# Kernel tuning notes

Hardware: AMD Instinct MI355X
Metric: run time of the kernel (lower is better)

Reference implementation:

```python
import jax
import jax.numpy as jnp
from jax import lax
import numpy as np

B, ND, H, W = 8, 8, 512, 512
CONF = 0.9
MARGIN = 3.0
MIN_CLUSTER = 50
MAX_X = 102.4
MPP0, MPP1 = 0.2, 0.2
K = 32  # max clusters (torch version grows an unbounded python list)


def setup_inputs() -> dict:
    key = jax.random.key(0)
    k1, k2, k3, k4, k5, k6 = jax.random.split(key, 6)
    return {
        "seg": jax.random.uniform(k1, (B, 1, H, W), dtype=jnp.float32),
        "embedding": jax.random.normal(k2, (B, ND, H, W), dtype=jnp.float32),
        "offset_pred": jax.random.normal(k3, (B, 1, H, W), dtype=jnp.float32),
        "z_pred": jax.random.normal(k4, (B, 1, H, W), dtype=jnp.float32),
        "intrinsic": jax.random.normal(k5, (B, 3, 3), dtype=jnp.float32),
        "extrinsic": jax.random.normal(k6, (B, 4, 4), dtype=jnp.float32),
    }


def _cluster_one(seg_flat, emb_flat):
    # seg_flat: [N], emb_flat: [N, ND]. Greedy sequential embedding clustering
    # (naive_cluster_nd): running-mean centers, assign to nearest center if
    # within MARGIN else open a new one. Fixed K slots; counts>0 marks active.
    nd = emb_flat.shape[1]

    def step(carry, xs):
        centers, counts = carry  # [K, nd], [K]
        s, e = xs
        valid = s >= CONF
        d = jnp.sqrt(jnp.sum((centers - e) ** 2, axis=1))
        d = jnp.where(counts > 0, d, jnp.inf)
        cid_min = jnp.argmin(d).astype(jnp.int32)
        join = d[cid_min] < MARGIN
        n_active = jnp.sum(counts > 0).astype(jnp.int32)
        cid = jnp.where(join, cid_min, jnp.minimum(n_active, K - 1))
        cnt = counts[cid]
        new_c = jnp.where(join, (centers[cid] * cnt + e) / (cnt + 1.0), e)
        centers = jnp.where(valid, centers.at[cid].set(new_c), centers)
        counts = jnp.where(valid, counts.at[cid].add(1.0), counts)
        return (centers, counts), jnp.where(valid, cid, -1)

    init = (jnp.zeros((K, nd), emb_flat.dtype), jnp.zeros((K,), emb_flat.dtype))
    (_, _), cids = lax.scan(step, init, (seg_flat, emb_flat))
    return cids  # [N] int32, -1 = background


def reference(seg, embedding, offset_pred, z_pred, intrinsic, extrinsic):
    b, nd, h, w = embedding.shape
    seg_flat = seg[:, 0].reshape(b, h * w)
    emb_flat = embedding.reshape(b, nd, h * w).transpose(0, 2, 1)  # [B, N, nd]
    cids = jax.vmap(_cluster_one)(seg_flat, emb_flat).reshape(b, h, w)
    lanes = jnp.where(cids >= 0, cids + 1, 0)  # [B, H, W], 0 = background

    # mean_col_by_row_with_offset_z: per (batch, lane, row) mean of col+offset and z
    offset_y = jax.nn.sigmoid(offset_pred[:, 0])          # [B, H, W]
    x_adj = jnp.arange(w, dtype=seg.dtype)[None, None, :] + offset_y
    zc = z_pred[:, 0]
    b_idx = jnp.arange(b)[:, None, None]
    h_idx = jnp.arange(h)[None, :, None]
    seg_ids = ((b_idx * (K + 1) + lanes) * h + h_idx).reshape(-1)
    num = b * (K + 1) * h

    def ssum(v):
        return jax.ops.segment_sum(v.reshape(-1), seg_ids, num_segments=num).reshape(b, K + 1, h)[:, 1:]

    cnt = ssum(jnp.ones((b, h, w), seg.dtype))            # [B, K, H]
    mean_x = ssum(x_adj) / jnp.maximum(cnt, 1.0)
    mean_z = ssum(zc) / jnp.maximum(cnt, 1.0)

    size = cnt.sum(-1)                                    # cluster pixel count
    n_rows = (cnt > 0).sum(-1)                            # rows per lane
    valid = (cnt > 0) & (size[:, :, None] >= MIN_CLUSTER) & (n_rows[:, :, None] >= 2)

    # ego-coordinate transform from forward()
    x_world = (MAX_X / MPP0 - (jnp.arange(h, dtype=seg.dtype) + 0.5)) * MPP0  # [H]
    x_world = jnp.broadcast_to(x_world, (b, K, h))
    y_world = -(mean_x - (w // 2)) * MPP1
    points = jnp.stack([x_world, y_world, mean_z], axis=1)  # [B, 3, K, H]
    points = jnp.where(valid[:, None], points, 0.0)
    return points, valid
```

## Files before the change

kernel.cpp:

```cpp
#include <hip/hip_runtime.h>

#define HW_ (512 * 512)
#define B_ 8
#define H_ 512
#define W_ 512
#define K_ 32
#define CH_ 16
#define CHPIX_ (HW_ / CH_)

__global__ void k_count(const float* __restrict__ seg, int* __restrict__ chunkCnt) {
  const int blk = blockIdx.x;
  const int t = threadIdx.x;
  const float4* __restrict__ s4 = (const float4*)(seg + (size_t)blk * CHPIX_) + (size_t)t * 16;
  int cnt = 0;
#pragma unroll
  for (int j = 0; j < 16; ++j) {
    float4 v = s4[j];
    cnt += (v.x >= 0.9f) + (v.y >= 0.9f) + (v.z >= 0.9f) + (v.w >= 0.9f);
  }
  __shared__ int red[256];
  red[t] = cnt;
  __syncthreads();
  for (int off = 128; off > 0; off >>= 1) {
    if (t < off) red[t] += red[t + off];
    __syncthreads();
  }
  if (t == 0) chunkCnt[blk] = red[0];
}

__global__ void k_scan(const int* __restrict__ chunkCnt, int* __restrict__ chunkBase,
                       int* __restrict__ nvalid, int cap) {
  const int t = threadIdx.x;
  if (t < B_ * CH_) {
    const int b = t / CH_, c = t % CH_;
    int base = 0;
    for (int q = 0; q < c; ++q) base += chunkCnt[b * CH_ + q];
    chunkBase[t] = base;
    if (c == CH_ - 1) nvalid[b] = min(base + chunkCnt[t], cap);
  }
}

__global__ void k_fill(const float* __restrict__ seg, const float* __restrict__ emb,
                       const int* __restrict__ chunkBase, unsigned char* __restrict__ lanes,
                       int* __restrict__ idxC, float* __restrict__ embC, int cap) {
  const int blk = blockIdx.x;
  const int b = blk / CH_;
  const int t = threadIdx.x;
  const size_t pixbase = (size_t)blk * CHPIX_ + (size_t)t * 64;
  const float4* __restrict__ s4 = (const float4*)(seg + pixbase);

  int cnt = 0;
#pragma unroll
  for (int j = 0; j < 16; ++j) {
    float4 v = s4[j];
    cnt += (v.x >= 0.9f) + (v.y >= 0.9f) + (v.z >= 0.9f) + (v.w >= 0.9f);
  }
  __shared__ int pre[256];
  pre[t] = cnt;
  __syncthreads();
  for (int off = 1; off < 256; off <<= 1) {
    int mine = pre[t];
    int add = (t >= off) ? pre[t - off] : 0;
    __syncthreads();
    pre[t] = mine + add;
    __syncthreads();
  }
  int w = chunkBase[blk] + pre[t] - cnt;

  uint4 z = {0u, 0u, 0u, 0u};
  uint4* lz = (uint4*)(lanes + pixbase);
  lz[0] = z; lz[1] = z; lz[2] = z; lz[3] = z;

  const float* __restrict__ eb = emb + (size_t)b * 8 * HW_;
  const int pixInB = (int)(pixbase - (size_t)b * HW_);
  for (int j = 0; j < 16; ++j) {
    float4 v = s4[j];
    float sv[4] = {v.x, v.y, v.z, v.w};
#pragma unroll
    for (int q = 0; q < 4; ++q) {
      if (sv[q] >= 0.9f && w < cap) {
        const int p = pixInB + j * 4 + q;
        idxC[(size_t)b * cap + w] = p;
        float* dst = embC + ((size_t)b * cap + w) * 8;
#pragma unroll
        for (int dd = 0; dd < 8; ++dd) dst[dd] = eb[(size_t)dd * HW_ + p];
        ++w;
      }
    }
  }
}


#define TILE_ 32

__device__ __forceinline__ void stage16(const float* g, float* l) {
  __builtin_amdgcn_global_load_lds(
      (const __attribute__((address_space(1))) void*)g,
      (__attribute__((address_space(3))) void*)l, 16, 0, 0);
}

#define RLF(V, L) __uint_as_float((unsigned)__builtin_amdgcn_readlane(__float_as_int(V), (L)))

#define STEPP(J)                                                                     \
  do {                                                                               \
    const float e0 = RLF(td.x, 2 * (J)), e1 = RLF(td.y, 2 * (J));                    \
    const float e2 = RLF(td.z, 2 * (J)), e3 = RLF(td.w, 2 * (J));                    \
    const float e4 = RLF(td.x, 2 * (J) + 1), e5 = RLF(td.y, 2 * (J) + 1);            \
    const float e6 = RLF(td.z, 2 * (J) + 1), e7 = RLF(td.w, 2 * (J) + 1);            \
    float t0 = C0 - e0, t1 = C1 - e1, t2 = C2 - e2, t3 = C3 - e3;                    \
    float t4 = C4 - e4, t5 = C5 - e5, t6 = C6 - e6, t7 = C7 - e7;                    \
    float a0 = t0 * t0 + t1 * t1;                                                    \
    float a1 = t2 * t2 + t3 * t3;                                                    \
    float a2 = t4 * t4 + t5 * t5;                                                    \
    float a3 = t6 * t6 + t7 * t7;                                                    \
    float dsq = (a0 + a1) + (a2 + a3);                                               \
    unsigned db = __float_as_uint(dsq);                                              \
    unsigned dbm = db > emptyBits ? db : emptyBits;         \
    unsigned key = (dbm & 0xFFFFFFE0u) | (unsigned)cl;             \
    unsigned mn = key, mr;                                                           \
    mr = (unsigned)__builtin_amdgcn_update_dpp(0, (int)mn, 0xB1, 0xF, 0xF, true);    \
    mn = mn < mr ? mn : mr;                                                          \
    mr = (unsigned)__builtin_amdgcn_update_dpp(0, (int)mn, 0x4E, 0xF, 0xF, true);    \
    mn = mn < mr ? mn : mr;                                                          \
    mr = (unsigned)__builtin_amdgcn_update_dpp(0, (int)mn, 0x141, 0xF, 0xF, true);   \
    mn = mn < mr ? mn : mr;                                                          \
    mr = (unsigned)__builtin_amdgcn_update_dpp(0, (int)mn, 0x140, 0xF, 0xF, true);   \
    mn = mn < mr ? mn : mr;                                                          \
    unsigned q0 = (unsigned)__builtin_amdgcn_readlane((int)mn, 0);                   \
    unsigned q1 = (unsigned)__builtin_amdgcn_readlane((int)mn, 16);                  \
    unsigned mv = q0 < q1 ? q0 : q1;                            \
    bool join = mv < 0x41100000u;            \
    int cid = join ? (int)(mv & 31u) : (nact < 31 ? nact : 31);                      \
    nact += join ? 0 : 1;                                                            \
    bool own = (cl == cid);                                                          \
    float wj = join ? inv : 1.0f;                                                    \
    float w = own ? wj : 0.0f;                                                       \
    C0 = __builtin_fmaf(t0, -w, C0);                                                 \
    C1 = __builtin_fmaf(t1, -w, C1);                                                 \
    C2 = __builtin_fmaf(t2, -w, C2);                                                 \
    C3 = __builtin_fmaf(t3, -w, C3);                                                 \
    C4 = __builtin_fmaf(t4, -w, C4);                                                 \
    C5 = __builtin_fmaf(t5, -w, C5);                                                 \
    C6 = __builtin_fmaf(t6, -w, C6);                                                 \
    C7 = __builtin_fmaf(t7, -w, C7);                                                 \
    cnt += own ? 1.0f : 0.0f;                                                        \
    inv = __builtin_amdgcn_rcpf(cnt + 1.0f);          \
    emptyBits = own ? 0u : emptyBits;                                                \
    pk |= (unsigned long long)(unsigned)(cid + 1) << (((J) & 7) * 8);                \
    if (((J) & 7) == 7) {                                                            \
      if (lane == 0) *(unsigned long long*)(cptr + ((J) & ~7)) = pk;                 \
      pk = 0ULL;                                                                     \
    }                                                                                \
  } while (0)

__global__ __launch_bounds__(64, 1) void k_cluster(const float* __restrict__ embC,
                                                   const int* __restrict__ nvalid,
                                                   unsigned char* __restrict__ cidArr,
                                                   int cap) {
  __shared__ float lds[512];
  const int b = blockIdx.x;
  const int lane = threadIdx.x;
  const int cl = lane & 31;
  const int n = nvalid[b];
  if (n <= 0) return;
  const int nTiles = (n + TILE_ - 1) / TILE_;

  const float* src = embC + (size_t)b * cap * 8 + lane * 4;
  unsigned char* cidB = cidArr + (size_t)b * HW_;

  float C0 = 0.f, C1 = 0.f, C2 = 0.f, C3 = 0.f, C4 = 0.f, C5 = 0.f, C6 = 0.f, C7 = 0.f;
  float cnt = 0.f, inv = 1.0f;
  unsigned emptyBits = 0x7F800000u;
  int nact = 0;
  unsigned long long pk = 0ULL;

  stage16(src, lds);
  asm volatile("s_waitcnt vmcnt(0)" ::: "memory");
  __builtin_amdgcn_sched_barrier(0);
  float4 td = ((const float4*)lds)[lane];

  for (int ti = 0; ti < nTiles; ++ti) {
    unsigned char* cptr = cidB + ti * TILE_;
    if (ti + 1 < nTiles)
      stage16(src + (size_t)(ti + 1) * 256, lds + ((ti + 1) & 1) * 128);

    STEPP(0);  STEPP(1);  STEPP(2);  STEPP(3);
    STEPP(4);  STEPP(5);  STEPP(6);  STEPP(7);
    STEPP(8);  STEPP(9);  STEPP(10); STEPP(11);
    STEPP(12); STEPP(13); STEPP(14); STEPP(15);
    STEPP(16); STEPP(17); STEPP(18); STEPP(19);
    STEPP(20); STEPP(21); STEPP(22); STEPP(23);
    STEPP(24); STEPP(25); STEPP(26); STEPP(27);
    STEPP(28); STEPP(29); STEPP(30); STEPP(31);

    if (ti + 1 < nTiles) {
      asm volatile("s_waitcnt vmcnt(4)" ::: "memory");
      __builtin_amdgcn_sched_barrier(0);
      td = ((const float4*)(lds + ((ti + 1) & 1) * 128))[lane];
    }
  }
}

__global__ void k_scatter(const unsigned char* __restrict__ cidArr,
                          const int* __restrict__ idxC, const int* __restrict__ nvalid,
                          unsigned char* __restrict__ lanes, int cap) {
  const int b = blockIdx.y;
  const int n = nvalid[b];
  for (int j = blockIdx.x * blockDim.x + threadIdx.x; j < n; j += gridDim.x * blockDim.x) {
    lanes[(size_t)b * HW_ + idxC[(size_t)b * cap + j]] = cidArr[(size_t)b * HW_ + j];
  }
}

__global__ void k_rowsum(const unsigned char* __restrict__ lanes,
                         const float* __restrict__ offp, const float* __restrict__ zp,
                         float* __restrict__ cnt, float* __restrict__ sx,
                         float* __restrict__ sz) {
  const int bh = blockIdx.x;
  const int b = bh >> 9, h = bh & 511;
  __shared__ float sc[33], sxx[33], szz[33];
  const int t = threadIdx.x;
  if (t < 33) { sc[t] = 0.f; sxx[t] = 0.f; szz[t] = 0.f; }
  __syncthreads();
  const size_t base = (size_t)bh * W_;
  for (int x = t; x < W_; x += 256) {
    int ln = lanes[base + x];
    float o = offp[base + x];
    float sig = 1.0f / (1.0f + expf(-o));
    float xa = (float)x + sig;
    float zv = zp[base + x];
    atomicAdd(&sc[ln], 1.0f);
    atomicAdd(&sxx[ln], xa);
    atomicAdd(&szz[ln], zv);
  }
  __syncthreads();
  if (t >= 1 && t < 33) {
    size_t o = ((size_t)b * K_ + (t - 1)) * H_ + h;
    cnt[o] = sc[t]; sx[o] = sxx[t]; sz[o] = szz[t];
  }
}

__global__ void k_final(const float* __restrict__ cnt, const float* __restrict__ sx,
                        const float* __restrict__ sz, float* __restrict__ out) {
  const int bk = blockIdx.x;
  const int b = bk >> 5, k = bk & 31;
  const int h = threadIdx.x;
  const size_t o = (size_t)bk * H_ + h;
  float c = cnt[o];
  float sc_ = c, sn = (c > 0.f) ? 1.f : 0.f;
#pragma unroll
  for (int off = 32; off >= 1; off >>= 1) {
    sc_ += __shfl_down(sc_, off);
    sn += __shfl_down(sn, off);
  }
  __shared__ float rs[8], rn[8], tot[2];
  const int wid = h >> 6, lid = h & 63;
  if (lid == 0) { rs[wid] = sc_; rn[wid] = sn; }
  __syncthreads();
  if (h == 0) {
    float a = 0, bb = 0;
#pragma unroll
    for (int q = 0; q < 8; ++q) { a += rs[q]; bb += rn[q]; }
    tot[0] = a; tot[1] = bb;
  }
  __syncthreads();
  float size = tot[0], nrows = tot[1];
  bool valid = (c > 0.f) && (size >= 50.f) && (nrows >= 2.f);
  float mx = sx[o] / fmaxf(c, 1.f);
  float mz = sz[o] / fmaxf(c, 1.f);
  float xw = (512.0f - ((float)h + 0.5f)) * 0.2f;
  float yw = -(mx - 256.0f) * 0.2f;
  out[((size_t)(b * 3 + 0) * K_ + k) * H_ + h] = valid ? xw : 0.f;
  out[((size_t)(b * 3 + 1) * K_ + k) * H_ + h] = valid ? yw : 0.f;
  out[((size_t)(b * 3 + 2) * K_ + k) * H_ + h] = valid ? mz : 0.f;
  out[(size_t)B_ * 3 * K_ * H_ + (size_t)bk * H_ + h] = valid ? 1.f : 0.f;
}

extern "C" void kernel_launch(void* const* d_in, const int* in_sizes, int n_in,
                              void* d_out, int out_size, void* d_ws, size_t ws_size,
                              hipStream_t stream) {
  const float* seg  = (const float*)d_in[0];
  const float* emb  = (const float*)d_in[1];
  const float* offp = (const float*)d_in[2];
  const float* zp   = (const float*)d_in[3];
  float* out = (float*)d_out;
  char* ws = (char*)d_ws;

  const size_t lanesOff = 0;
  const size_t cntOff   = (size_t)B_ * HW_;
  const size_t sxOff    = cntOff + (size_t)B_ * K_ * H_ * 4;
  const size_t szOff    = sxOff  + (size_t)B_ * K_ * H_ * 4;
  const size_t nvOff    = szOff  + (size_t)B_ * K_ * H_ * 4;
  const size_t ccOff    = nvOff + 256;
  const size_t cbOff    = ccOff + 1024;
  const size_t cidOff   = cbOff + 1024;
  const size_t idxOff   = cidOff + (size_t)B_ * HW_;
  size_t avail = (ws_size > idxOff + 4096) ? (ws_size - idxOff - 4096) : 0;
  long long capLL = (long long)(avail / ((size_t)B_ * 36));
  if (capLL > (long long)HW_) capLL = HW_;
  if (capLL < 1) capLL = 1;
  const int cap = (int)capLL;
  const size_t embOff = idxOff + (size_t)B_ * cap * 4;

  unsigned char* lanes = (unsigned char*)(ws + lanesOff);
  float* cnt = (float*)(ws + cntOff);
  float* sx  = (float*)(ws + sxOff);
  float* sz  = (float*)(ws + szOff);
  int* nvalid = (int*)(ws + nvOff);
  int* chunkCnt  = (int*)(ws + ccOff);
  int* chunkBase = (int*)(ws + cbOff);
  unsigned char* cidArr = (unsigned char*)(ws + cidOff);
  int* idxC   = (int*)(ws + idxOff);
  float* embC = (float*)(ws + embOff);

  k_count<<<B_ * CH_, 256, 0, stream>>>(seg, chunkCnt);
  k_scan<<<1, 128, 0, stream>>>(chunkCnt, chunkBase, nvalid, cap);
  k_fill<<<B_ * CH_, 256, 0, stream>>>(seg, emb, chunkBase, lanes, idxC, embC, cap);
  k_cluster<<<B_, 64, 0, stream>>>(embC, nvalid, cidArr, cap);
  k_scatter<<<dim3(64, B_), 256, 0, stream>>>(cidArr, idxC, nvalid, lanes, cap);
  k_rowsum<<<B_ * H_, 256, 0, stream>>>(lanes, offp, zp, cnt, sx, sz);
  k_final<<<B_ * K_, H_, 0, stream>>>(cnt, sx, sz, out);
}
```

Measured before the change: 3.119 ms.

## Pack two batches per wave in clustering kernel with fused DPP min reduction

The greedy clustering kernel now processes two batch images in one 64-lane wave: each 32-lane half holds the cluster centers for one image, and the grid shrinks from eight blocks to four. The cross-lane min reduction is rewritten in inline assembly as fused v_min_u32_dpp instructions, aiming to shorten the serial per-pixel dependency chain. Tiles shrink to 16 pixels per phase, and each step does twice as many readlanes plus per-half selects. Each wave now runs for the longer of its two images, and the shorter image computes on padding data past its end.

```diff
diff --git a/kernel.cpp b/kernel.cpp
--- a/kernel.cpp
+++ b/kernel.cpp
@@ -91,7 +91,7 @@
 }
 
 
-#define TILE_ 32
+#define PHPX_ 16
 
 __device__ __forceinline__ void stage16(const float* g, float* l) {
   __builtin_amdgcn_global_load_lds(
@@ -100,57 +100,78 @@
 }
 
 #define RLF(V, L) __uint_as_float((unsigned)__builtin_amdgcn_readlane(__float_as_int(V), (L)))
-
-#define STEPP(J)                                                                     \
-  do {                                                                               \
-    const float e0 = RLF(td.x, 2 * (J)), e1 = RLF(td.y, 2 * (J));                    \
-    const float e2 = RLF(td.z, 2 * (J)), e3 = RLF(td.w, 2 * (J));                    \
-    const float e4 = RLF(td.x, 2 * (J) + 1), e5 = RLF(td.y, 2 * (J) + 1);            \
-    const float e6 = RLF(td.z, 2 * (J) + 1), e7 = RLF(td.w, 2 * (J) + 1);            \
-    float t0 = C0 - e0, t1 = C1 - e1, t2 = C2 - e2, t3 = C3 - e3;                    \
-    float t4 = C4 - e4, t5 = C5 - e5, t6 = C6 - e6, t7 = C7 - e7;                    \
-    float a0 = t0 * t0 + t1 * t1;                                                    \
-    float a1 = t2 * t2 + t3 * t3;                                                    \
-    float a2 = t4 * t4 + t5 * t5;                                                    \
-    float a3 = t6 * t6 + t7 * t7;                                                    \
-    float dsq = (a0 + a1) + (a2 + a3);                                               \
-    unsigned db = __float_as_uint(dsq);                                              \
-    unsigned dbm = db > emptyBits ? db : emptyBits;         \
-    unsigned key = (dbm & 0xFFFFFFE0u) | (unsigned)cl;             \
-    unsigned mn = key, mr;                                                           \
-    mr = (unsigned)__builtin_amdgcn_update_dpp(0, (int)mn, 0xB1, 0xF, 0xF, true);    \
-    mn = mn < mr ? mn : mr;                                                          \
-    mr = (unsigned)__builtin_amdgcn_update_dpp(0, (int)mn, 0x4E, 0xF, 0xF, true);    \
-    mn = mn < mr ? mn : mr;                                                          \
-    mr = (unsigned)__builtin_amdgcn_update_dpp(0, (int)mn, 0x141, 0xF, 0xF, true);   \
-    mn = mn < mr ? mn : mr;                                                          \
-    mr = (unsigned)__builtin_amdgcn_update_dpp(0, (int)mn, 0x140, 0xF, 0xF, true);   \
-    mn = mn < mr ? mn : mr;                                                          \
-    unsigned q0 = (unsigned)__builtin_amdgcn_readlane((int)mn, 0);                   \
-    unsigned q1 = (unsigned)__builtin_amdgcn_readlane((int)mn, 16);                  \
-    unsigned mv = q0 < q1 ? q0 : q1;                            \
-    bool join = mv < 0x41100000u;            \
-    int cid = join ? (int)(mv & 31u) : (nact < 31 ? nact : 31);                      \
-    nact += join ? 0 : 1;                                                            \
-    bool own = (cl == cid);                                                          \
-    float wj = join ? inv : 1.0f;                                                    \
-    float w = own ? wj : 0.0f;                                                       \
-    C0 = __builtin_fmaf(t0, -w, C0);                                                 \
-    C1 = __builtin_fmaf(t1, -w, C1);                                                 \
-    C2 = __builtin_fmaf(t2, -w, C2);                                                 \
-    C3 = __builtin_fmaf(t3, -w, C3);                                                 \
-    C4 = __builtin_fmaf(t4, -w, C4);                                                 \
-    C5 = __builtin_fmaf(t5, -w, C5);                                                 \
-    C6 = __builtin_fmaf(t6, -w, C6);                                                 \
-    C7 = __builtin_fmaf(t7, -w, C7);                                                 \
-    cnt += own ? 1.0f : 0.0f;                                                        \
-    inv = __builtin_amdgcn_rcpf(cnt + 1.0f);          \
-    emptyBits = own ? 0u : emptyBits;                                                \
-    pk |= (unsigned long long)(unsigned)(cid + 1) << (((J) & 7) * 8);                \
-    if (((J) & 7) == 7) {                                                            \
-      if (lane == 0) *(unsigned long long*)(cptr + ((J) & ~7)) = pk;                 \
-      pk = 0ULL;                                                                     \
-    }                                                                                \
+#define RLU(V, L) ((unsigned)__builtin_amdgcn_readlane((int)(V), (L)))
+
+#define PSTEP(J)                                                                   \
+  do {                                                                             \
+    const float eA0 = RLF(td.x, 2 * (J)), eA1 = RLF(td.y, 2 * (J));                \
+    const float eA2 = RLF(td.z, 2 * (J)), eA3 = RLF(td.w, 2 * (J));                \
+    const float eA4 = RLF(td.x, 2 * (J) + 1), eA5 = RLF(td.y, 2 * (J) + 1);        \
+    const float eA6 = RLF(td.z, 2 * (J) + 1), eA7 = RLF(td.w, 2 * (J) + 1);        \
+    const float eB0 = RLF(td.x, 32 + 2 * (J)), eB1 = RLF(td.y, 32 + 2 * (J));      \
+    const float eB2 = RLF(td.z, 32 + 2 * (J)), eB3 = RLF(td.w, 32 + 2 * (J));      \
+    const float eB4 = RLF(td.x, 33 + 2 * (J)), eB5 = RLF(td.y, 33 + 2 * (J));      \
+    const float eB6 = RLF(td.z, 33 + 2 * (J)), eB7 = RLF(td.w, 33 + 2 * (J));      \
+    float t0 = hi ? (C0 - eB0) : (C0 - eA0);                                       \
+    float t1 = hi ? (C1 - eB1) : (C1 - eA1);                                       \
+    float t2 = hi ? (C2 - eB2) : (C2 - eA2);                                       \
+    float t3 = hi ? (C3 - eB3) : (C3 - eA3);                                       \
+    float t4 = hi ? (C4 - eB4) : (C4 - eA4);                                       \
+    float t5 = hi ? (C5 - eB5) : (C5 - eA5);                                       \
+    float t6 = hi ? (C6 - eB6) : (C6 - eA6);                                       \
+    float t7 = hi ? (C7 - eB7) : (C7 - eA7);                                       \
+    float a0 = t0 * t0 + t1 * t1;                                                  \
+    float a1 = t2 * t2 + t3 * t3;                                                  \
+    float a2 = t4 * t4 + t5 * t5;                                                  \
+    float a3 = t6 * t6 + t7 * t7;                                                  \
+    float dsq = (a0 + a1) + (a2 + a3);                                             \
+    unsigned db = __float_as_uint(dsq);                                            \
+    unsigned dbm = db > emptyBits ? db : emptyBits;       \
+    unsigned mn = (dbm & 0xFFFFFFE0u) | (unsigned)cl;                              \
+    asm volatile(                                                                  \
+        "s_nop 1\n\t"                                                              \
+        "v_min_u32_dpp %0, %0, %0 quad_perm:[1,0,3,2] row_mask:0xf bank_mask:0xf\n\t" \
+        "s_nop 1\n\t"                                                              \
+        "v_min_u32_dpp %0, %0, %0 quad_perm:[2,3,0,1] row_mask:0xf bank_mask:0xf\n\t" \
+        "s_nop 1\n\t"                                                              \
+        "v_min_u32_dpp %0, %0, %0 row_half_mirror row_mask:0xf bank_mask:0xf\n\t"  \
+        "s_nop 1\n\t"                                                              \
+        "v_min_u32_dpp %0, %0, %0 row_mirror row_mask:0xf bank_mask:0xf\n\t"       \
+        "s_nop 1"                                                                  \
+        : "+v"(mn));                                                               \
+    unsigned q0 = RLU(mn, 0), q1 = RLU(mn, 16);                                    \
+    unsigned q2 = RLU(mn, 32), q3 = RLU(mn, 48);                                   \
+    unsigned mvA = q0 < q1 ? q0 : q1;                         \
+    unsigned mvB = q2 < q3 ? q2 : q3;                                              \
+    bool joinA = mvA < 0x41100000u;               \
+    bool joinB = mvB < 0x41100000u;                                                \
+    int cidA = joinA ? (int)(mvA & 31u) : (nactA < 31 ? nactA : 31);               \
+    int cidB = joinB ? (int)(mvB & 31u) : (nactB < 31 ? nactB : 31);               \
+    nactA += joinA ? 0 : 1;                                                        \
+    nactB += joinB ? 0 : 1;                                                        \
+    bool own = (cl == (hi ? cidB : cidA));                                         \
+    bool join_my = hi ? joinB : joinA;                                             \
+    float wj = join_my ? inv : 1.0f;                                               \
+    float w = own ? wj : 0.0f;                                                     \
+    C0 = __builtin_fmaf(t0, -w, C0);                                               \
+    C1 = __builtin_fmaf(t1, -w, C1);                                               \
+    C2 = __builtin_fmaf(t2, -w, C2);                                               \
+    C3 = __builtin_fmaf(t3, -w, C3);                                               \
+    C4 = __builtin_fmaf(t4, -w, C4);                                               \
+    C5 = __builtin_fmaf(t5, -w, C5);                                               \
+    C6 = __builtin_fmaf(t6, -w, C6);                                               \
+    C7 = __builtin_fmaf(t7, -w, C7);                                               \
+    cnt += own ? 1.0f : 0.0f;                                                      \
+    inv = __builtin_amdgcn_rcpf(cnt + 1.0f);        \
+    emptyBits = own ? 0u : emptyBits;                                              \
+    pkA |= (unsigned long long)(unsigned)(cidA + 1) << (((J) & 7) * 8);            \
+    pkB |= (unsigned long long)(unsigned)(cidB + 1) << (((J) & 7) * 8);            \
+    if (((J) & 7) == 7) {                                                          \
+      if (lane == 0) *(unsigned long long*)(cpA + ((J) & ~7)) = pkA;               \
+      if (lane == 32) *(unsigned long long*)(cpB + ((J) & ~7)) = pkB;              \
+      pkA = 0ULL;                                                                  \
+      pkB = 0ULL;                                                                  \
+    }                                                                              \
   } while (0)
 
 __global__ __launch_bounds__(64, 1) void k_cluster(const float* __restrict__ embC,
@@ -158,45 +179,46 @@
                                                    unsigned char* __restrict__ cidArr,
                                                    int cap) {
   __shared__ float lds[512];
-  const int b = blockIdx.x;
+  const int blk = blockIdx.x;
   const int lane = threadIdx.x;
+  const bool hi = lane >= 32;
   const int cl = lane & 31;
-  const int n = nvalid[b];
-  if (n <= 0) return;
-  const int nTiles = (n + TILE_ - 1) / TILE_;
-
-  const float* src = embC + (size_t)b * cap * 8 + lane * 4;
-  unsigned char* cidB = cidArr + (size_t)b * HW_;
+  const int bA = 2 * blk, bB = 2 * blk + 1;
+  const int nA = nvalid[bA], nB = nvalid[bB];
+  const int nMax = nA > nB ? nA : nB;
+  if (nMax <= 0) return;
+  const int nPh = (nMax + PHPX_ - 1) / PHPX_;
+
+  const float* gsrc = embC + (size_t)(hi ? bB : bA) * cap * 8 + (size_t)cl * 4;
+  unsigned char* cA = cidArr + (size_t)bA * HW_;
+  unsigned char* cB = cidArr + (size_t)bB * HW_;
 
   float C0 = 0.f, C1 = 0.f, C2 = 0.f, C3 = 0.f, C4 = 0.f, C5 = 0.f, C6 = 0.f, C7 = 0.f;
   float cnt = 0.f, inv = 1.0f;
   unsigned emptyBits = 0x7F800000u;
-  int nact = 0;
-  unsigned long long pk = 0ULL;
-
-  stage16(src, lds);
+  int nactA = 0, nactB = 0;
+  unsigned long long pkA = 0ULL, pkB = 0ULL;
+
+  stage16(gsrc, lds);
   asm volatile("s_waitcnt vmcnt(0)" ::: "memory");
   __builtin_amdgcn_sched_barrier(0);
   float4 td = ((const float4*)lds)[lane];
 
-  for (int ti = 0; ti < nTiles; ++ti) {
-    unsigned char* cptr = cidB + ti * TILE_;
-    if (ti + 1 < nTiles)
-      stage16(src + (size_t)(ti + 1) * 256, lds + ((ti + 1) & 1) * 128);
-
-    STEPP(0);  STEPP(1);  STEPP(2);  STEPP(3);
-    STEPP(4);  STEPP(5);  STEPP(6);  STEPP(7);
-    STEPP(8);  STEPP(9);  STEPP(10); STEPP(11);
-    STEPP(12); STEPP(13); STEPP(14); STEPP(15);
-    STEPP(16); STEPP(17); STEPP(18); STEPP(19);
-    STEPP(20); STEPP(21); STEPP(22); STEPP(23);
-    STEPP(24); STEPP(25); STEPP(26); STEPP(27);
-    STEPP(28); STEPP(29); STEPP(30); STEPP(31);
-
-    if (ti + 1 < nTiles) {
+  for (int ph = 0; ph < nPh; ++ph) {
+    unsigned char* cpA = cA + ph * PHPX_;
+    unsigned char* cpB = cB + ph * PHPX_;
+    if (ph + 1 < nPh)
+      stage16(gsrc + (size_t)(ph + 1) * 128, lds + ((ph + 1) & 1) * 256);
+
+    PSTEP(0);  PSTEP(1);  PSTEP(2);  PSTEP(3);
+    PSTEP(4);  PSTEP(5);  PSTEP(6);  PSTEP(7);
+    PSTEP(8);  PSTEP(9);  PSTEP(10); PSTEP(11);
+    PSTEP(12); PSTEP(13); PSTEP(14); PSTEP(15);
+
+    if (ph + 1 < nPh) {
       asm volatile("s_waitcnt vmcnt(4)" ::: "memory");
       __builtin_amdgcn_sched_barrier(0);
-      td = ((const float4*)(lds + ((ti + 1) & 1) * 128))[lane];
+      td = ((const float4*)(lds + ((ph + 1) & 1) * 256))[lane];
     }
   }
 }
@@ -294,10 +316,11 @@
   const size_t cbOff    = ccOff + 1024;
   const size_t cidOff   = cbOff + 1024;
   const size_t idxOff   = cidOff + (size_t)B_ * HW_;
-  size_t avail = (ws_size > idxOff + 4096) ? (ws_size - idxOff - 4096) : 0;
+  size_t avail = (ws_size > idxOff + 8192) ? (ws_size - idxOff - 8192) : 0;
   long long capLL = (long long)(avail / ((size_t)B_ * 36));
   if (capLL > (long long)HW_) capLL = HW_;
-  if (capLL < 1) capLL = 1;
+  if (capLL < 2) capLL = 2;
+  capLL &= ~1LL;
   const int cap = (int)capLL;
   const size_t embOff = idxOff + (size_t)B_ * cap * 4;
 
@@ -315,7 +338,7 @@
   k_count<<<B_ * CH_, 256, 0, stream>>>(seg, chunkCnt);
   k_scan<<<1, 128, 0, stream>>>(chunkCnt, chunkBase, nvalid, cap);
   k_fill<<<B_ * CH_, 256, 0, stream>>>(seg, emb, chunkBase, lanes, idxC, embC, cap);
-  k_cluster<<<B_, 64, 0, stream>>>(embC, nvalid, cidArr, cap);
+  k_cluster<<<B_ / 2, 64, 0, stream>>>(embC, nvalid, cidArr, cap);
   k_scatter<<<dim3(64, B_), 256, 0, stream>>>(cidArr, idxC, nvalid, lanes, cap);
   k_rowsum<<<B_ * H_, 256, 0, stream>>>(lanes, offp, zp, cnt, sx, sz);
   k_final<<<B_ * K_, H_, 0, stream>>>(cnt, sx, sz, out);
```

Measured after the change: 6.262 ms. 101% more time.

## Feed cluster embeddings via scalar loads instead of LDS staging and readlane

Applied to the files above, without the earlier changes.

The sequential clustering kernel now loads each point's 8-dim embedding straight into scalar registers with s_load_dwordx16, double-buffered eight points at a time. This replaces the global-to-LDS staging followed by per-element readlane broadcasts, removing eight readlanes and the LDS traffic from every serial step. It also flips the delta sign so the distance uses fma, and writes the packed cluster ids every eight points. The change adds prefetch reads past the valid range, so the workspace padding and an even cap are adjusted to keep them in bounds.

```diff
diff --git a/kernel.cpp b/kernel.cpp
--- a/kernel.cpp
+++ b/kernel.cpp
@@ -91,33 +91,40 @@
 }
 
 
-#define TILE_ 32
-
-__device__ __forceinline__ void stage16(const float* g, float* l) {
-  __builtin_amdgcn_global_load_lds(
-      (const __attribute__((address_space(1))) void*)g,
-      (__attribute__((address_space(3))) void*)l, 16, 0, 0);
-}
-
-#define RLF(V, L) __uint_as_float((unsigned)__builtin_amdgcn_readlane(__float_as_int(V), (L)))
-
-#define STEPP(J)                                                                     \
+typedef unsigned u32x16 __attribute__((ext_vector_type(16)));
+
+#define RLU(V, L) ((unsigned)__builtin_amdgcn_readlane((int)(V), (L)))
+
+#define SLOAD(SA, SB, OFF)                                            \
+  asm volatile("s_load_dwordx16 %0, %2, %3\n\t"                       \
+               "s_load_dwordx16 %1, %2, %4"                           \
+               : "=s"(SA), "=s"(SB)                                   \
+               : "s"(src), "s"((OFF)), "s"((OFF) + 64u));
+
+#define SWAIT(SA, SB) \
+  asm volatile("s_waitcnt lgkmcnt(0)" : "+s"(SA), "+s"(SB));
+
+#define STEPS(J, SV, BI)                                                              \
   do {                                                                               \
-    const float e0 = RLF(td.x, 2 * (J)), e1 = RLF(td.y, 2 * (J));                    \
-    const float e2 = RLF(td.z, 2 * (J)), e3 = RLF(td.w, 2 * (J));                    \
-    const float e4 = RLF(td.x, 2 * (J) + 1), e5 = RLF(td.y, 2 * (J) + 1);            \
-    const float e6 = RLF(td.z, 2 * (J) + 1), e7 = RLF(td.w, 2 * (J) + 1);            \
-    float t0 = C0 - e0, t1 = C1 - e1, t2 = C2 - e2, t3 = C3 - e3;                    \
-    float t4 = C4 - e4, t5 = C5 - e5, t6 = C6 - e6, t7 = C7 - e7;                    \
-    float a0 = t0 * t0 + t1 * t1;                                                    \
-    float a1 = t2 * t2 + t3 * t3;                                                    \
-    float a2 = t4 * t4 + t5 * t5;                                                    \
-    float a3 = t6 * t6 + t7 * t7;                                                    \
-    float dsq = (a0 + a1) + (a2 + a3);                                               \
+    const float e0 = __uint_as_float((SV)[(BI) + 0]);                                \
+    const float e1 = __uint_as_float((SV)[(BI) + 1]);                                \
+    const float e2 = __uint_as_float((SV)[(BI) + 2]);                                \
+    const float e3 = __uint_as_float((SV)[(BI) + 3]);                                \
+    const float e4 = __uint_as_float((SV)[(BI) + 4]);                                \
+    const float e5 = __uint_as_float((SV)[(BI) + 5]);                                \
+    const float e6 = __uint_as_float((SV)[(BI) + 6]);                                \
+    const float e7 = __uint_as_float((SV)[(BI) + 7]);                                \
+    float t0 = e0 - C0, t1 = e1 - C1, t2 = e2 - C2, t3 = e3 - C3;                    \
+    float t4 = e4 - C4, t5 = e5 - C5, t6 = e6 - C6, t7 = e7 - C7;                    \
+    float m0 = t0 * t0; m0 = __builtin_fmaf(t1, t1, m0);                             \
+    float m1 = t2 * t2; m1 = __builtin_fmaf(t3, t3, m1);                             \
+    float m2 = t4 * t4; m2 = __builtin_fmaf(t5, t5, m2);                             \
+    float m3 = t6 * t6; m3 = __builtin_fmaf(t7, t7, m3);                             \
+    float dsq = (m0 + m1) + (m2 + m3);                                               \
     unsigned db = __float_as_uint(dsq);                                              \
     unsigned dbm = db > emptyBits ? db : emptyBits;         \
-    unsigned key = (dbm & 0xFFFFFFE0u) | (unsigned)cl;             \
-    unsigned mn = key, mr;                                                           \
+    unsigned mn = (dbm & 0xFFFFFFE0u) | (unsigned)cl;      \
+    unsigned mr;                                                                     \
     mr = (unsigned)__builtin_amdgcn_update_dpp(0, (int)mn, 0xB1, 0xF, 0xF, true);    \
     mn = mn < mr ? mn : mr;                                                          \
     mr = (unsigned)__builtin_amdgcn_update_dpp(0, (int)mn, 0x4E, 0xF, 0xF, true);    \
@@ -126,8 +133,7 @@
     mn = mn < mr ? mn : mr;                                                          \
     mr = (unsigned)__builtin_amdgcn_update_dpp(0, (int)mn, 0x140, 0xF, 0xF, true);   \
     mn = mn < mr ? mn : mr;                                                          \
-    unsigned q0 = (unsigned)__builtin_amdgcn_readlane((int)mn, 0);                   \
-    unsigned q1 = (unsigned)__builtin_amdgcn_readlane((int)mn, 16);                  \
+    unsigned q0 = RLU(mn, 0), q1 = RLU(mn, 16);                                      \
     unsigned mv = q0 < q1 ? q0 : q1;                            \
     bool join = mv < 0x41100000u;            \
     int cid = join ? (int)(mv & 31u) : (nact < 31 ? nact : 31);                      \
@@ -135,37 +141,31 @@
     bool own = (cl == cid);                                                          \
     float wj = join ? inv : 1.0f;                                                    \
     float w = own ? wj : 0.0f;                                                       \
-    C0 = __builtin_fmaf(t0, -w, C0);                                                 \
-    C1 = __builtin_fmaf(t1, -w, C1);                                                 \
-    C2 = __builtin_fmaf(t2, -w, C2);                                                 \
-    C3 = __builtin_fmaf(t3, -w, C3);                                                 \
-    C4 = __builtin_fmaf(t4, -w, C4);                                                 \
-    C5 = __builtin_fmaf(t5, -w, C5);                                                 \
-    C6 = __builtin_fmaf(t6, -w, C6);                                                 \
-    C7 = __builtin_fmaf(t7, -w, C7);                                                 \
+    C0 = __builtin_fmaf(t0, w, C0);                       \
+    C1 = __builtin_fmaf(t1, w, C1);                                                  \
+    C2 = __builtin_fmaf(t2, w, C2);                                                  \
+    C3 = __builtin_fmaf(t3, w, C3);                                                  \
+    C4 = __builtin_fmaf(t4, w, C4);                                                  \
+    C5 = __builtin_fmaf(t5, w, C5);                                                  \
+    C6 = __builtin_fmaf(t6, w, C6);                                                  \
+    C7 = __builtin_fmaf(t7, w, C7);                                                  \
     cnt += own ? 1.0f : 0.0f;                                                        \
     inv = __builtin_amdgcn_rcpf(cnt + 1.0f);          \
     emptyBits = own ? 0u : emptyBits;                                                \
-    pk |= (unsigned long long)(unsigned)(cid + 1) << (((J) & 7) * 8);                \
-    if (((J) & 7) == 7) {                                                            \
-      if (lane == 0) *(unsigned long long*)(cptr + ((J) & ~7)) = pk;                 \
-      pk = 0ULL;                                                                     \
-    }                                                                                \
+    pk |= (unsigned long long)(unsigned)(cid + 1) << ((J) * 8);                      \
   } while (0)
 
 __global__ __launch_bounds__(64, 1) void k_cluster(const float* __restrict__ embC,
                                                    const int* __restrict__ nvalid,
                                                    unsigned char* __restrict__ cidArr,
                                                    int cap) {
-  __shared__ float lds[512];
   const int b = blockIdx.x;
   const int lane = threadIdx.x;
   const int cl = lane & 31;
   const int n = nvalid[b];
   if (n <= 0) return;
-  const int nTiles = (n + TILE_ - 1) / TILE_;
-
-  const float* src = embC + (size_t)b * cap * 8 + lane * 4;
+
+  const float* src = embC + (size_t)b * cap * 8;
   unsigned char* cidB = cidArr + (size_t)b * HW_;
 
   float C0 = 0.f, C1 = 0.f, C2 = 0.f, C3 = 0.f, C4 = 0.f, C5 = 0.f, C6 = 0.f, C7 = 0.f;
@@ -174,30 +174,24 @@
   int nact = 0;
   unsigned long long pk = 0ULL;
 
-  stage16(src, lds);
-  asm volatile("s_waitcnt vmcnt(0)" ::: "memory");
-  __builtin_amdgcn_sched_barrier(0);
-  float4 td = ((const float4*)lds)[lane];
-
-  for (int ti = 0; ti < nTiles; ++ti) {
-    unsigned char* cptr = cidB + ti * TILE_;
-    if (ti + 1 < nTiles)
-      stage16(src + (size_t)(ti + 1) * 256, lds + ((ti + 1) & 1) * 128);
-
-    STEPP(0);  STEPP(1);  STEPP(2);  STEPP(3);
-    STEPP(4);  STEPP(5);  STEPP(6);  STEPP(7);
-    STEPP(8);  STEPP(9);  STEPP(10); STEPP(11);
-    STEPP(12); STEPP(13); STEPP(14); STEPP(15);
-    STEPP(16); STEPP(17); STEPP(18); STEPP(19);
-    STEPP(20); STEPP(21); STEPP(22); STEPP(23);
-    STEPP(24); STEPP(25); STEPP(26); STEPP(27);
-    STEPP(28); STEPP(29); STEPP(30); STEPP(31);
-
-    if (ti + 1 < nTiles) {
-      asm volatile("s_waitcnt vmcnt(4)" ::: "memory");
-      __builtin_amdgcn_sched_barrier(0);
-      td = ((const float4*)(lds + ((ti + 1) & 1) * 128))[lane];
-    }
+  u32x16 a0, b0, a1, b1;
+  SLOAD(a0, b0, 0u);
+  SWAIT(a0, b0);
+  SLOAD(a1, b1, 128u);
+  unsigned offNext = 256u;
+
+  const int nOct = (n + 7) >> 3;
+  for (int o = 0; o < nOct; ++o) {
+    STEPS(0, a0, 0); STEPS(1, a0, 8); STEPS(2, b0, 0); STEPS(3, b0, 8);
+    SWAIT(a1, b1);
+    SLOAD(a0, b0, offNext);
+    offNext += 128u;
+    STEPS(4, a1, 0); STEPS(5, a1, 8); STEPS(6, b1, 0); STEPS(7, b1, 8);
+    if (lane == 0) *(unsigned long long*)(cidB + o * 8) = pk;
+    pk = 0ULL;
+    SWAIT(a0, b0);
+    SLOAD(a1, b1, offNext);
+    offNext += 128u;
   }
 }
 
@@ -294,10 +288,11 @@
   const size_t cbOff    = ccOff + 1024;
   const size_t cidOff   = cbOff + 1024;
   const size_t idxOff   = cidOff + (size_t)B_ * HW_;
-  size_t avail = (ws_size > idxOff + 4096) ? (ws_size - idxOff - 4096) : 0;
+  size_t avail = (ws_size > idxOff + 8192) ? (ws_size - idxOff - 8192) : 0;
   long long capLL = (long long)(avail / ((size_t)B_ * 36));
   if (capLL > (long long)HW_) capLL = HW_;
-  if (capLL < 1) capLL = 1;
+  if (capLL < 2) capLL = 2;
+  capLL &= ~1LL;
   const int cap = (int)capLL;
   const size_t embOff = idxOff + (size_t)B_ * cap * 4;
 
```

New measurement: 3.971 ms. 1.27x slower.

## Speculate next-step distance algebraically to shorten serial clustering dependency chain

Applied to the files above, without the earlier changes.

Rewrites the sequential clustering step so the next pixel's squared distance is computed ahead of the centre update. It uses the identity |e - C'|^2 = |e - C|^2 - 2w·g + w^2·|t|^2, which takes the centre update off the critical path of the loop-carried chain. The tile is doubled to 64 pixels with two-stage staging, and per-tile cluster ids are written as four 16-byte stores. The reassociated float arithmetic can change rounding, so join decisions near the margin may flip.

```diff
diff --git a/kernel.cpp b/kernel.cpp
--- a/kernel.cpp
+++ b/kernel.cpp
@@ -91,7 +91,7 @@
 }
 
 
-#define TILE_ 32
+#define TILE_ 64
 
 __device__ __forceinline__ void stage16(const float* g, float* l) {
   __builtin_amdgcn_global_load_lds(
@@ -100,64 +100,68 @@
 }
 
 #define RLF(V, L) __uint_as_float((unsigned)__builtin_amdgcn_readlane(__float_as_int(V), (L)))
-
-#define STEPP(J)                                                                     \
-  do {                                                                               \
-    const float e0 = RLF(td.x, 2 * (J)), e1 = RLF(td.y, 2 * (J));                    \
-    const float e2 = RLF(td.z, 2 * (J)), e3 = RLF(td.w, 2 * (J));                    \
-    const float e4 = RLF(td.x, 2 * (J) + 1), e5 = RLF(td.y, 2 * (J) + 1);            \
-    const float e6 = RLF(td.z, 2 * (J) + 1), e7 = RLF(td.w, 2 * (J) + 1);            \
-    float t0 = C0 - e0, t1 = C1 - e1, t2 = C2 - e2, t3 = C3 - e3;                    \
-    float t4 = C4 - e4, t5 = C5 - e5, t6 = C6 - e6, t7 = C7 - e7;                    \
-    float a0 = t0 * t0 + t1 * t1;                                                    \
-    float a1 = t2 * t2 + t3 * t3;                                                    \
-    float a2 = t4 * t4 + t5 * t5;                                                    \
-    float a3 = t6 * t6 + t7 * t7;                                                    \
-    float dsq = (a0 + a1) + (a2 + a3);                                               \
-    unsigned db = __float_as_uint(dsq);                                              \
-    unsigned dbm = db > emptyBits ? db : emptyBits;         \
-    unsigned key = (dbm & 0xFFFFFFE0u) | (unsigned)cl;             \
-    unsigned mn = key, mr;                                                           \
-    mr = (unsigned)__builtin_amdgcn_update_dpp(0, (int)mn, 0xB1, 0xF, 0xF, true);    \
-    mn = mn < mr ? mn : mr;                                                          \
-    mr = (unsigned)__builtin_amdgcn_update_dpp(0, (int)mn, 0x4E, 0xF, 0xF, true);    \
-    mn = mn < mr ? mn : mr;                                                          \
-    mr = (unsigned)__builtin_amdgcn_update_dpp(0, (int)mn, 0x141, 0xF, 0xF, true);   \
-    mn = mn < mr ? mn : mr;                                                          \
-    mr = (unsigned)__builtin_amdgcn_update_dpp(0, (int)mn, 0x140, 0xF, 0xF, true);   \
-    mn = mn < mr ? mn : mr;                                                          \
-    unsigned q0 = (unsigned)__builtin_amdgcn_readlane((int)mn, 0);                   \
-    unsigned q1 = (unsigned)__builtin_amdgcn_readlane((int)mn, 16);                  \
-    unsigned mv = q0 < q1 ? q0 : q1;                            \
-    bool join = mv < 0x41100000u;            \
-    int cid = join ? (int)(mv & 31u) : (nact < 31 ? nact : 31);                      \
-    nact += join ? 0 : 1;                                                            \
-    bool own = (cl == cid);                                                          \
-    float wj = join ? inv : 1.0f;                                                    \
-    float w = own ? wj : 0.0f;                                                       \
-    C0 = __builtin_fmaf(t0, -w, C0);                                                 \
-    C1 = __builtin_fmaf(t1, -w, C1);                                                 \
-    C2 = __builtin_fmaf(t2, -w, C2);                                                 \
-    C3 = __builtin_fmaf(t3, -w, C3);                                                 \
-    C4 = __builtin_fmaf(t4, -w, C4);                                                 \
-    C5 = __builtin_fmaf(t5, -w, C5);                                                 \
-    C6 = __builtin_fmaf(t6, -w, C6);                                                 \
-    C7 = __builtin_fmaf(t7, -w, C7);                                                 \
-    cnt += own ? 1.0f : 0.0f;                                                        \
-    inv = __builtin_amdgcn_rcpf(cnt + 1.0f);          \
-    emptyBits = own ? 0u : emptyBits;                                                \
-    pk |= (unsigned long long)(unsigned)(cid + 1) << (((J) & 7) * 8);                \
-    if (((J) & 7) == 7) {                                                            \
-      if (lane == 0) *(unsigned long long*)(cptr + ((J) & ~7)) = pk;                 \
-      pk = 0ULL;                                                                     \
-    }                                                                                \
+#define RLU(V, L) ((unsigned)__builtin_amdgcn_readlane((int)(V), (L)))
+#define DPPMIN(CTRL)                                                                  \
+  {                                                                                   \
+    unsigned mr_ = (unsigned)__builtin_amdgcn_update_dpp(0, (int)mn, CTRL, 0xF, 0xF, true); \
+    mn = mn < mr_ ? mn : mr_;                                                         \
+  }
+
+#define STEPX(PK, SH, TD, L)                                                     \
+  do {                                                                           \
+                                        \
+    float dsq = __builtin_fmaf(wp, __builtin_fmaf(wp, dsqq, m2g), dspec);        \
+    unsigned db = __float_as_uint(dsq);                                          \
+    unsigned dbm = db > emptyBits ? db : emptyBits;     \
+    unsigned mn = (dbm & 0xFFFFFFE0u) | (unsigned)cl;                            \
+    DPPMIN(0xB1) DPPMIN(0x4E) DPPMIN(0x141) DPPMIN(0x140)                        \
+    unsigned q0 = RLU(mn, 0), q1 = RLU(mn, 16);                                  \
+    unsigned mv = q0 < q1 ? q0 : q1;                        \
+    bool join = mv < 0x41100000u;               \
+    int cid = join ? (int)(mv & 31u) : (nact < 31 ? nact : 31);                  \
+    nact += join ? 0 : 1;                                                        \
+    bool own = (cl == cid);                                                      \
+    float wj = join ? inv : 1.0f;                                                \
+    float w = own ? wj : 0.0f;                                                   \
+                 \
+    C0 = __builtin_fmaf(wp, t0, C0); C1 = __builtin_fmaf(wp, t1, C1);            \
+    C2 = __builtin_fmaf(wp, t2, C2); C3 = __builtin_fmaf(wp, t3, C3);            \
+    C4 = __builtin_fmaf(wp, t4, C4); C5 = __builtin_fmaf(wp, t5, C5);            \
+    C6 = __builtin_fmaf(wp, t6, C6); C7 = __builtin_fmaf(wp, t7, C7);            \
+    t0 = __builtin_fmaf(-wp, t0, s0); t1 = __builtin_fmaf(-wp, t1, s1);          \
+    t2 = __builtin_fmaf(-wp, t2, s2); t3 = __builtin_fmaf(-wp, t3, s3);          \
+    t4 = __builtin_fmaf(-wp, t4, s4); t5 = __builtin_fmaf(-wp, t5, s5);          \
+    t6 = __builtin_fmaf(-wp, t6, s6); t7 = __builtin_fmaf(-wp, t7, s7);          \
+                    \
+    const float e0n = RLF((TD).x, (L)), e1n = RLF((TD).y, (L));                  \
+    const float e2n = RLF((TD).z, (L)), e3n = RLF((TD).w, (L));                  \
+    const float e4n = RLF((TD).x, (L) + 1), e5n = RLF((TD).y, (L) + 1);          \
+    const float e6n = RLF((TD).z, (L) + 1), e7n = RLF((TD).w, (L) + 1);          \
+    s0 = e0n - C0; s1 = e1n - C1; s2 = e2n - C2; s3 = e3n - C3;                  \
+    s4 = e4n - C4; s5 = e5n - C5; s6 = e6n - C6; s7 = e7n - C7;                  \
+    float p0 = s0 * s0; p0 = __builtin_fmaf(s1, s1, p0);                         \
+    float p1 = s2 * s2; p1 = __builtin_fmaf(s3, s3, p1);                         \
+    float p2 = s4 * s4; p2 = __builtin_fmaf(s5, s5, p2);                         \
+    float p3 = s6 * s6; p3 = __builtin_fmaf(s7, s7, p3);                         \
+    dspec = (p0 + p1) + (p2 + p3);                                               \
+    float gg = t0 * s0; gg = __builtin_fmaf(t1, s1, gg);                         \
+    gg = __builtin_fmaf(t2, s2, gg); gg = __builtin_fmaf(t3, s3, gg);            \
+    gg = __builtin_fmaf(t4, s4, gg); gg = __builtin_fmaf(t5, s5, gg);            \
+    gg = __builtin_fmaf(t6, s6, gg); gg = __builtin_fmaf(t7, s7, gg);            \
+    m2g = -2.0f * gg;                                                            \
+    dsqq = dsq;                                                                  \
+    wp = w;                                                                      \
+    cnt += own ? 1.0f : 0.0f;                                                    \
+    inv = __builtin_amdgcn_rcpf(cnt + 1.0f);                 \
+    emptyBits = own ? 0u : emptyBits;                                            \
+    PK |= (unsigned long long)(unsigned)(cid + 1) << ((SH) * 8);                 \
   } while (0)
 
 __global__ __launch_bounds__(64, 1) void k_cluster(const float* __restrict__ embC,
                                                    const int* __restrict__ nvalid,
                                                    unsigned char* __restrict__ cidArr,
                                                    int cap) {
-  __shared__ float lds[512];
+  __shared__ float lds[1024];
   const int b = blockIdx.x;
   const int lane = threadIdx.x;
   const int cl = lane & 31;
@@ -167,37 +171,82 @@
 
   const float* src = embC + (size_t)b * cap * 8 + lane * 4;
   unsigned char* cidB = cidArr + (size_t)b * HW_;
+  const float4* f4 = (const float4*)lds;
 
   float C0 = 0.f, C1 = 0.f, C2 = 0.f, C3 = 0.f, C4 = 0.f, C5 = 0.f, C6 = 0.f, C7 = 0.f;
-  float cnt = 0.f, inv = 1.0f;
+  float t0 = 0.f, t1 = 0.f, t2 = 0.f, t3 = 0.f, t4 = 0.f, t5 = 0.f, t6 = 0.f, t7 = 0.f;
+  float s0, s1, s2, s3, s4, s5, s6, s7;
+  float cnt = 0.f, inv = 1.0f, wp = 0.f, m2g = 0.f, dsqq = 0.f, dspec;
   unsigned emptyBits = 0x7F800000u;
   int nact = 0;
-  unsigned long long pk = 0ULL;
+  unsigned long long pk0 = 0, pk1 = 0, pk2 = 0, pk3 = 0, pk4 = 0, pk5 = 0, pk6 = 0, pk7 = 0;
 
   stage16(src, lds);
+  stage16(src + 256, lds + 256);
   asm volatile("s_waitcnt vmcnt(0)" ::: "memory");
   __builtin_amdgcn_sched_barrier(0);
-  float4 td = ((const float4*)lds)[lane];
+  float4 td = f4[lane], td2 = f4[64 + lane];
+  float4 tdN = td, td2N = td2;
+
+  s0 = RLF(td.x, 0); s1 = RLF(td.y, 0); s2 = RLF(td.z, 0); s3 = RLF(td.w, 0);
+  s4 = RLF(td.x, 1); s5 = RLF(td.y, 1); s6 = RLF(td.z, 1); s7 = RLF(td.w, 1);
+  {
+    float p0 = s0 * s0 + s1 * s1, p1 = s2 * s2 + s3 * s3;
+    float p2 = s4 * s4 + s5 * s5, p3 = s6 * s6 + s7 * s7;
+    dspec = (p0 + p1) + (p2 + p3);
+  }
 
   for (int ti = 0; ti < nTiles; ++ti) {
-    unsigned char* cptr = cidB + ti * TILE_;
-    if (ti + 1 < nTiles)
-      stage16(src + (size_t)(ti + 1) * 256, lds + ((ti + 1) & 1) * 128);
-
-    STEPP(0);  STEPP(1);  STEPP(2);  STEPP(3);
-    STEPP(4);  STEPP(5);  STEPP(6);  STEPP(7);
-    STEPP(8);  STEPP(9);  STEPP(10); STEPP(11);
-    STEPP(12); STEPP(13); STEPP(14); STEPP(15);
-    STEPP(16); STEPP(17); STEPP(18); STEPP(19);
-    STEPP(20); STEPP(21); STEPP(22); STEPP(23);
-    STEPP(24); STEPP(25); STEPP(26); STEPP(27);
-    STEPP(28); STEPP(29); STEPP(30); STEPP(31);
-
-    if (ti + 1 < nTiles) {
-      asm volatile("s_waitcnt vmcnt(4)" ::: "memory");
+    const bool more = (ti + 1 < nTiles);
+    if (more) {
+      stage16(src + (size_t)(ti + 1) * 512, lds + ((ti + 1) & 1) * 512);
+      stage16(src + (size_t)(ti + 1) * 512 + 256, lds + ((ti + 1) & 1) * 512 + 256);
+    }
+    STEPX(pk0, 0, td, 2);   STEPX(pk0, 1, td, 4);   STEPX(pk0, 2, td, 6);   STEPX(pk0, 3, td, 8);
+    STEPX(pk0, 4, td, 10);  STEPX(pk0, 5, td, 12);  STEPX(pk0, 6, td, 14);  STEPX(pk0, 7, td, 16);
+    STEPX(pk1, 0, td, 18);  STEPX(pk1, 1, td, 20);  STEPX(pk1, 2, td, 22);  STEPX(pk1, 3, td, 24);
+    STEPX(pk1, 4, td, 26);  STEPX(pk1, 5, td, 28);  STEPX(pk1, 6, td, 30);  STEPX(pk1, 7, td, 32);
+    STEPX(pk2, 0, td, 34);  STEPX(pk2, 1, td, 36);  STEPX(pk2, 2, td, 38);  STEPX(pk2, 3, td, 40);
+    STEPX(pk2, 4, td, 42);  STEPX(pk2, 5, td, 44);  STEPX(pk2, 6, td, 46);  STEPX(pk2, 7, td, 48);
+    STEPX(pk3, 0, td, 50);  STEPX(pk3, 1, td, 52);  STEPX(pk3, 2, td, 54);  STEPX(pk3, 3, td, 56);
+    STEPX(pk3, 4, td, 58);  STEPX(pk3, 5, td, 60);  STEPX(pk3, 6, td, 62);  STEPX(pk4, 0, td2, 0);
+    STEPX(pk4, 1, td2, 2);  STEPX(pk4, 2, td2, 4);  STEPX(pk4, 3, td2, 6);  STEPX(pk4, 4, td2, 8);
+    STEPX(pk4, 5, td2, 10); STEPX(pk4, 6, td2, 12); STEPX(pk4, 7, td2, 14); STEPX(pk5, 0, td2, 16);
+    STEPX(pk5, 1, td2, 18); STEPX(pk5, 2, td2, 20); STEPX(pk5, 3, td2, 22); STEPX(pk5, 4, td2, 24);
+    STEPX(pk5, 5, td2, 26); STEPX(pk5, 6, td2, 28); STEPX(pk5, 7, td2, 30); STEPX(pk6, 0, td2, 32);
+
+    if (more) {
+      asm volatile("s_waitcnt vmcnt(0)" ::: "memory");
       __builtin_amdgcn_sched_barrier(0);
-      td = ((const float4*)(lds + ((ti + 1) & 1) * 128))[lane];
-    }
+      const int ph = ((ti + 1) & 1) * 128;
+      tdN = f4[ph + lane];
+      td2N = f4[ph + 64 + lane];
+    }
+    STEPX(pk6, 1, td2, 34); STEPX(pk6, 2, td2, 36); STEPX(pk6, 3, td2, 38); STEPX(pk6, 4, td2, 40);
+    STEPX(pk6, 5, td2, 42); STEPX(pk6, 6, td2, 44); STEPX(pk6, 7, td2, 46); STEPX(pk7, 0, td2, 48);
+    STEPX(pk7, 1, td2, 50); STEPX(pk7, 2, td2, 52); STEPX(pk7, 3, td2, 54); STEPX(pk7, 4, td2, 56);
+    STEPX(pk7, 5, td2, 58); STEPX(pk7, 6, td2, 60); STEPX(pk7, 7, td2, 62); STEPX(pk0, 0, tdN, 0);
+    (void)0;
+
+    if (lane == 0) {
+      unsigned char* cptr = cidB + ti * TILE_;
+      uint4 v;
+      v.x = (unsigned)pk0; v.y = (unsigned)(pk0 >> 32);
+      v.z = (unsigned)pk1; v.w = (unsigned)(pk1 >> 32);
+      *(uint4*)(cptr + 0) = v;
+      v.x = (unsigned)pk2; v.y = (unsigned)(pk2 >> 32);
+      v.z = (unsigned)pk3; v.w = (unsigned)(pk3 >> 32);
+      *(uint4*)(cptr + 16) = v;
+      v.x = (unsigned)pk4; v.y = (unsigned)(pk4 >> 32);
+      v.z = (unsigned)pk5; v.w = (unsigned)(pk5 >> 32);
+      *(uint4*)(cptr + 32) = v;
+      v.x = (unsigned)pk6; v.y = (unsigned)(pk6 >> 32);
+      v.z = (unsigned)pk7; v.w = (unsigned)(pk7 >> 32);
+      *(uint4*)(cptr + 48) = v;
+    }
+    pk0 = pk1 = pk2 = pk3 = pk4 = pk5 = pk6 = pk7 = 0ULL;
+    td = tdN;
+    td2 = td2N;
   }
 }
 
@@ -275,6 +324,95 @@
   out[(size_t)B_ * 3 * K_ * H_ + (size_t)bk * H_ + h] = valid ? 1.f : 0.f;
 }
 
+__global__ __launch_bounds__(64, 1) void k_cluster2(const float* __restrict__ embC,
+                                                    const int* __restrict__ nvalid,
+                                                    unsigned char* __restrict__ cidArr,
+                                                    int cap) {
+  __shared__ float lds[1024];
+  const int b = blockIdx.x;
+  const int lane = threadIdx.x;
+  const int cl = lane & 31;
+  const int n = nvalid[b];
+  if (n <= 0) return;
+  const int nTiles = (n + TILE_ - 1) / TILE_;
+
+  const float* src = embC + (size_t)b * cap * 8 + lane * 4;
+  unsigned char* cidB = cidArr + (size_t)b * HW_;
+  const float4* f4 = (const float4*)lds;
+
+  float C0 = 0.f, C1 = 0.f, C2 = 0.f, C3 = 0.f, C4 = 0.f, C5 = 0.f, C6 = 0.f, C7 = 0.f;
+  float t0 = 0.f, t1 = 0.f, t2 = 0.f, t3 = 0.f, t4 = 0.f, t5 = 0.f, t6 = 0.f, t7 = 0.f;
+  float s0, s1, s2, s3, s4, s5, s6, s7;
+  float cnt = 0.f, inv = 1.0f, wp = 0.f, m2g = 0.f, dsqq = 0.f, dspec;
+  unsigned emptyBits = 0x7F800000u;
+  int nact = 0;
+  unsigned long long pk0 = 0, pk1 = 0, pk2 = 0, pk3 = 0, pk4 = 0, pk5 = 0, pk6 = 0, pk7 = 0;
+
+  stage16(src, lds);
+  stage16(src + 256, lds + 256);
+  asm volatile("s_waitcnt vmcnt(0)" ::: "memory");
+  __builtin_amdgcn_sched_barrier(0);
+  float4 td = f4[lane], td2 = f4[64 + lane];
+  float4 tdN = td, td2N = td2;
+
+  s0 = RLF(td.x, 0); s1 = RLF(td.y, 0); s2 = RLF(td.z, 0); s3 = RLF(td.w, 0);
+  s4 = RLF(td.x, 1); s5 = RLF(td.y, 1); s6 = RLF(td.z, 1); s7 = RLF(td.w, 1);
+  {
+    float p0 = s0 * s0 + s1 * s1, p1 = s2 * s2 + s3 * s3;
+    float p2 = s4 * s4 + s5 * s5, p3 = s6 * s6 + s7 * s7;
+    dspec = (p0 + p1) + (p2 + p3);
+  }
+
+#define ROW8(PK, S0, TDa, La, TDb, Lb, TDc, Lc, TDd, Ld, TDe, Le, TDf, Lf, TDg, Lg, TDh, Lh) \
+  STEPX(PK, 0, TDa, La); STEPX(PK, 1, TDb, Lb); STEPX(PK, 2, TDc, Lc); STEPX(PK, 3, TDd, Ld); \
+  STEPX(PK, 4, TDe, Le); STEPX(PK, 5, TDf, Lf); STEPX(PK, 6, TDg, Lg); STEPX(PK, 7, TDh, Lh);
+
+  for (int ti = 0; ti < nTiles; ++ti) {
+    const bool more = (ti + 1 < nTiles);
+    if (more) {
+      stage16(src + (size_t)(ti + 1) * 512, lds + ((ti + 1) & 1) * 512);
+      stage16(src + (size_t)(ti + 1) * 512 + 256, lds + ((ti + 1) & 1) * 512 + 256);
+    }
+    ROW8(pk0, 0, td, 2, td, 4, td, 6, td, 8, td, 10, td, 12, td, 14, td, 16)
+    ROW8(pk1, 8, td, 18, td, 20, td, 22, td, 24, td, 26, td, 28, td, 30, td, 32)
+    ROW8(pk2, 16, td, 34, td, 36, td, 38, td, 40, td, 42, td, 44, td, 46, td, 48)
+    ROW8(pk3, 24, td, 50, td, 52, td, 54, td, 56, td, 58, td, 60, td, 62, td2, 0)
+    ROW8(pk4, 32, td2, 2, td2, 4, td2, 6, td2, 8, td2, 10, td2, 12, td2, 14, td2, 16)
+    ROW8(pk5, 40, td2, 18, td2, 20, td2, 22, td2, 24, td2, 26, td2, 28, td2, 30, td2, 32)
+
+    if (more) {
+      asm volatile("s_waitcnt vmcnt(0)" ::: "memory");
+      __builtin_amdgcn_sched_barrier(0);
+      const int ph = ((ti + 1) & 1) * 128;
+      tdN = f4[ph + lane];
+      td2N = f4[ph + 64 + lane];
+    }
+    ROW8(pk6, 48, td2, 34, td2, 36, td2, 38, td2, 40, td2, 42, td2, 44, td2, 46, td2, 48)
+    ROW8(pk7, 56, td2, 50, td2, 52, td2, 54, td2, 56, td2, 58, td2, 60, td2, 62, tdN, 0)
+
+    if (lane == 0) {
+      unsigned char* cptr = cidB + ti * TILE_;
+      uint4 v;
+      v.x = (unsigned)pk0; v.y = (unsigned)(pk0 >> 32);
+      v.z = (unsigned)pk1; v.w = (unsigned)(pk1 >> 32);
+      *(uint4*)(cptr + 0) = v;
+      v.x = (unsigned)pk2; v.y = (unsigned)(pk2 >> 32);
+      v.z = (unsigned)pk3; v.w = (unsigned)(pk3 >> 32);
+      *(uint4*)(cptr + 16) = v;
+      v.x = (unsigned)pk4; v.y = (unsigned)(pk4 >> 32);
+      v.z = (unsigned)pk5; v.w = (unsigned)(pk5 >> 32);
+      *(uint4*)(cptr + 32) = v;
+      v.x = (unsigned)pk6; v.y = (unsigned)(pk6 >> 32);
+      v.z = (unsigned)pk7; v.w = (unsigned)(pk7 >> 32);
+      *(uint4*)(cptr + 48) = v;
+    }
+    pk0 = pk1 = pk2 = pk3 = pk4 = pk5 = pk6 = pk7 = 0ULL;
+    td = tdN;
+    td2 = td2N;
+  }
+#undef ROW8
+}
+
 extern "C" void kernel_launch(void* const* d_in, const int* in_sizes, int n_in,
                               void* d_out, int out_size, void* d_ws, size_t ws_size,
                               hipStream_t stream) {
@@ -294,10 +432,11 @@
   const size_t cbOff    = ccOff + 1024;
   const size_t cidOff   = cbOff + 1024;
   const size_t idxOff   = cidOff + (size_t)B_ * HW_;
-  size_t avail = (ws_size > idxOff + 4096) ? (ws_size - idxOff - 4096) : 0;
+  size_t avail = (ws_size > idxOff + 16384) ? (ws_size - idxOff - 16384) : 0;
   long long capLL = (long long)(avail / ((size_t)B_ * 36));
   if (capLL > (long long)HW_) capLL = HW_;
-  if (capLL < 1) capLL = 1;
+  if (capLL < 2) capLL = 2;
+  capLL &= ~1LL;
   const int cap = (int)capLL;
   const size_t embOff = idxOff + (size_t)B_ * cap * 4;
 
@@ -315,7 +454,7 @@
   k_count<<<B_ * CH_, 256, 0, stream>>>(seg, chunkCnt);
   k_scan<<<1, 128, 0, stream>>>(chunkCnt, chunkBase, nvalid, cap);
   k_fill<<<B_ * CH_, 256, 0, stream>>>(seg, emb, chunkBase, lanes, idxC, embC, cap);
-  k_cluster<<<B_, 64, 0, stream>>>(embC, nvalid, cidArr, cap);
+  k_cluster2<<<B_, 64, 0, stream>>>(embC, nvalid, cidArr, cap);
   k_scatter<<<dim3(64, B_), 256, 0, stream>>>(cidArr, idxC, nvalid, lanes, cap);
   k_rowsum<<<B_ * H_, 256, 0, stream>>>(lanes, offp, zp, cnt, sx, sz);
   k_final<<<B_ * K_, H_, 0, stream>>>(cnt, sx, sz, out);
```

Result: slower. 3.525 ms (+13.0%).
